# Optimization experiments

Measured on AMD Instinct MI355X. Metric: run time of the kernel, lower is better.

Reference implementation:

```python
import jax, jax.numpy as jnp
import numpy as np

NC, ND = 1024, 64        # computation nodes, device nodes
EC, ED = 16384, 1024     # edges in each graph
FC, FD = 128, 32         # raw feature dims
H = 1024                 # num_hidden
RH = 256                 # num_rnn_hidden


def gconv(feat, src, dst, n_nodes, W, b, act):
    """DGL GraphConv with edge-feature concat (edge feat == ones[E,1])."""
    e = src.shape[0]
    ones_e = jnp.ones((e,), feat.dtype)
    out_deg = jnp.clip(jax.ops.segment_sum(ones_e, src, num_segments=n_nodes), 1.0)
    feat_n = feat * (out_deg ** -0.5)[:, None]
    # sum distributes over concat columns: aggregate src feats and edge feats separately
    h_src = jax.ops.segment_sum(feat_n[src], dst, num_segments=n_nodes)      # [N, in]
    h_e = jax.ops.segment_sum(ones_e, dst, num_segments=n_nodes)[:, None]    # [N, 1]
    h = jnp.concatenate([h_src, h_e], axis=1)                                 # [N, in+1]
    rst = h @ W
    in_deg = jnp.clip(jax.ops.segment_sum(ones_e, dst, num_segments=n_nodes), 1.0)
    rst = rst * (in_deg ** -0.5)[:, None] + b
    return act(rst) if act is not None else rst


def gru_dir(x, Wx, Wh, b, reverse):
    """Keras GRU (reset_after=True), x: [B,T,D] -> [B,T,H]."""
    B = x.shape[0]
    h_dim = Wh.shape[0]
    b_in, b_rec = b[0], b[1]
    xp = jnp.einsum('btd,dh->bth', x, Wx) + b_in   # [B,T,3H]
    xs = jnp.swapaxes(xp, 0, 1)                    # [T,B,3H]
    if reverse:
        xs = xs[::-1]

    def step(h, xt):
        rec = h @ Wh + b_rec
        xz, xr, xh = jnp.split(xt, 3, axis=-1)
        rz, rr, rh = jnp.split(rec, 3, axis=-1)
        z = jax.nn.sigmoid(xz + rz)
        r = jax.nn.sigmoid(xr + rr)
        hh = jnp.tanh(xh + r * rh)
        h_new = z * h + (1.0 - z) * hh
        return h_new, h_new

    h0 = jnp.zeros((B, h_dim), x.dtype)
    _, ys = jax.lax.scan(step, h0, xs)
    if reverse:
        ys = ys[::-1]
    return jnp.swapaxes(ys, 0, 1)


def setup_inputs() -> dict:
    key = jax.random.key(0)
    ks = jax.random.split(key, 20)
    s = 0.05
    return {
        'comp_feat': jax.random.normal(ks[0], (NC, FC), jnp.float32),
        'dev_feat': jax.random.normal(ks[1], (ND, FD), jnp.float32),
        'comp_src': jax.random.randint(ks[2], (EC,), 0, NC, jnp.int32),
        'comp_dst': jax.random.randint(ks[3], (EC,), 0, NC, jnp.int32),
        'dev_src': jax.random.randint(ks[4], (ED,), 0, ND, jnp.int32),
        'dev_dst': jax.random.randint(ks[5], (ED,), 0, ND, jnp.int32),
        'W1c': jax.random.normal(ks[6], (FC + 1, H), jnp.float32) * s,
        'b1c': jnp.zeros((H,), jnp.float32),
        'W2c': jax.random.normal(ks[7], (H + 1, H), jnp.float32) * s,
        'b2c': jnp.zeros((H,), jnp.float32),
        'W1d': jax.random.normal(ks[8], (FD + 1, H), jnp.float32) * s,
        'b1d': jnp.zeros((H,), jnp.float32),
        'W2d': jax.random.normal(ks[9], (H + 1, H), jnp.float32) * s,
        'b2d': jnp.zeros((H,), jnp.float32),
        'Wx_f': jax.random.normal(ks[10], (2 * H, 3 * RH), jnp.float32) * s,
        'Wh_f': jax.random.normal(ks[11], (RH, 3 * RH), jnp.float32) * s,
        'b_f': jnp.zeros((2, 3 * RH), jnp.float32),
        'Wx_b': jax.random.normal(ks[12], (2 * H, 3 * RH), jnp.float32) * s,
        'Wh_b': jax.random.normal(ks[13], (RH, 3 * RH), jnp.float32) * s,
        'b_b': jnp.zeros((2, 3 * RH), jnp.float32),
        'Wf': jax.random.normal(ks[14], (2 * RH, 3), jnp.float32) * s,
        'bf': jnp.zeros((3,), jnp.float32),
    }


def reference(comp_feat, dev_feat, comp_src, comp_dst, dev_src, dev_dst,
              W1c, b1c, W2c, b2c, W1d, b1d, W2d, b2d,
              Wx_f, Wh_f, b_f, Wx_b, Wh_b, b_b, Wf, bf):
    # computation graph GConv stack
    x = gconv(comp_feat, comp_src, comp_dst, NC, W1c, b1c, jax.nn.elu)
    comp_emb = gconv(x, comp_src, comp_dst, NC, W2c, b2c, None)          # [NC, H]
    # device graph GConv stack
    x = gconv(dev_feat, dev_src, dev_dst, ND, W1d, b1d, jax.nn.elu)
    dev_emb = gconv(x, dev_src, dev_dst, ND, W2d, b2d, None)             # [ND, H]
    # pairwise concat: [NC, ND, 2H]
    c = jnp.broadcast_to(comp_emb[:, None, :], (NC, ND, H))
    d = jnp.broadcast_to(dev_emb[None, :, :], (NC, ND, H))
    x = jnp.concatenate([c, d], axis=-1)
    # bidirectional GRU over device axis
    yf = gru_dir(x, Wx_f, Wh_f, b_f, reverse=False)
    yb = gru_dir(x, Wx_b, Wh_b, b_b, reverse=True)
    y = jnp.concatenate([yf, yb], axis=-1)                               # [NC, ND, 2*RH]
    return jax.nn.log_softmax(y @ Wf + bf, axis=-1)                      # [NC, ND, 3]
```

## Files before the change

kernel.cpp:

```cpp
#include <hip/hip_runtime.h>
#include <math.h>

#define NCN 1024
#define NDN 64
#define ECE 16384
#define EDE 1024
#define FCF 128
#define FDF 32
#define HDIM 1024
#define RH 256
#define NG 768
#define TT 64

#define OFF_DEG_OC 0
#define OFF_DEG_IC 1024
#define OFF_DEG_OD 2048
#define OFF_DEG_ID 2112
#define OFF_AGG_C  2176
#define SZ_AGG_C   (1024*1028)
#define OFF_X1C    (OFF_AGG_C + SZ_AGG_C)
#define OFF_EMB_C  (OFF_X1C + 1024*1024)
#define OFF_AGG_D  (OFF_EMB_C + 1024*1024)
#define SZ_AGG_D   (64*1028)
#define OFF_X1D    (OFF_AGG_D + SZ_AGG_D)
#define OFF_EMB_D  (OFF_X1D + 64*1024)
#define OFF_AX     (OFF_EMB_D + 64*1024)
#define OFF_DX     (OFF_AX + 2*1024*768)
#define OFF_WHB    (OFF_DX + 2*64*768)

#define EPI_NONE 0
#define EPI_BIAS 1
#define EPI_GCONV 2
#define EPI_GCONV_ELU 3

typedef __attribute__((ext_vector_type(8))) short s16x8;
typedef __attribute__((ext_vector_type(4))) float f32x4;

__device__ __forceinline__ unsigned short bf16rne(float x) {
    unsigned u = __float_as_uint(x);
    return (unsigned short)((u + 0x7FFFu + ((u >> 16) & 1u)) >> 16);
}

__global__ void fill_k(float* p, int n, float v) {
    int i = blockIdx.x * blockDim.x + threadIdx.x;
    int stride = gridDim.x * blockDim.x;
    for (; i < n; i += stride) p[i] = v;
}

__global__ void degree_k(const int* __restrict__ csrc, const int* __restrict__ cdst,
                         const int* __restrict__ dsrc, const int* __restrict__ ddst,
                         float* ws) {
    int i = blockIdx.x * blockDim.x + threadIdx.x;
    if (i < ECE) {
        atomicAdd(&ws[OFF_DEG_OC + csrc[i]], 1.0f);
        atomicAdd(&ws[OFF_DEG_IC + cdst[i]], 1.0f);
    } else if (i < ECE + EDE) {
        int e = i - ECE;
        atomicAdd(&ws[OFF_DEG_OD + dsrc[e]], 1.0f);
        atomicAdd(&ws[OFF_DEG_ID + ddst[e]], 1.0f);
    }
}

__global__ void agg_k(const float* __restrict__ feat, int F, int logF,
                      const int* __restrict__ src, const int* __restrict__ dst,
                      int E, const float* __restrict__ degout,
                      float* __restrict__ agg, int lda) {
    int i = blockIdx.x * blockDim.x + threadIdx.x;
    int total = E << logF;
    if (i >= total) return;
    int e = i >> logF;
    int f = i & (F - 1);
    int s = src[e];
    float nv = feat[(s << logF) + f] * rsqrtf(fmaxf(degout[s], 1.0f));
    atomicAdd(&agg[dst[e] * lda + f], nv);
}

__global__ void degcol_k(float* agg, int lda, int F, const float* __restrict__ degin, int n) {
    int i = blockIdx.x * blockDim.x + threadIdx.x;
    if (i < n) agg[i * lda + F] = degin[i];
}

__global__ __launch_bounds__(256)
void gemm_k(const float* __restrict__ A, int lda,
            const float* __restrict__ B, int ldb,
            float* __restrict__ C, int ldc,
            int M, int N, int K, int epi,
            const float* __restrict__ scale, const float* __restrict__ bias) {
    __shared__ float As[16][68];
    __shared__ float Bs[16][64];
    int t = threadIdx.x;
    int tx = t & 15, ty = t >> 4;
    int row0 = blockIdx.y * 64, col0 = blockIdx.x * 64;
    int ar = t & 63, ac4 = t >> 6;
    int bk = t >> 4, bc4 = t & 15;
    float acc[4][4] = {};
    int ktiles = (K + 15) >> 4;
    bool avec = ((lda & 3) == 0);
    for (int kt = 0; kt < ktiles; ++kt) {
        int k0 = kt << 4;
        bool full = (k0 + 16 <= K);
        if (full && avec) {
            float4 av = *(const float4*)(A + (size_t)(row0 + ar) * lda + k0 + ac4 * 4);
            As[ac4 * 4 + 0][ar] = av.x; As[ac4 * 4 + 1][ar] = av.y;
            As[ac4 * 4 + 2][ar] = av.z; As[ac4 * 4 + 3][ar] = av.w;
        } else {
#pragma unroll
            for (int j = 0; j < 4; ++j) {
                int kc = k0 + ac4 * 4 + j;
                As[ac4 * 4 + j][ar] = (kc < K) ? A[(size_t)(row0 + ar) * lda + kc] : 0.0f;
            }
        }
        if (full) {
            float4 bv = *(const float4*)(B + (size_t)(k0 + bk) * ldb + col0 + bc4 * 4);
            *(float4*)&Bs[bk][bc4 * 4] = bv;
        } else {
            int kr = k0 + bk;
#pragma unroll
            for (int j = 0; j < 4; ++j)
                Bs[bk][bc4 * 4 + j] = (kr < K) ? B[(size_t)kr * ldb + col0 + bc4 * 4 + j] : 0.0f;
        }
        __syncthreads();
#pragma unroll
        for (int kk = 0; kk < 16; ++kk) {
            float4 a = *(const float4*)&As[kk][ty * 4];
            float4 b = *(const float4*)&Bs[kk][tx * 4];
            acc[0][0] += a.x * b.x; acc[0][1] += a.x * b.y; acc[0][2] += a.x * b.z; acc[0][3] += a.x * b.w;
            acc[1][0] += a.y * b.x; acc[1][1] += a.y * b.y; acc[1][2] += a.y * b.z; acc[1][3] += a.y * b.w;
            acc[2][0] += a.z * b.x; acc[2][1] += a.z * b.y; acc[2][2] += a.z * b.z; acc[2][3] += a.z * b.w;
            acc[3][0] += a.w * b.x; acc[3][1] += a.w * b.y; acc[3][2] += a.w * b.z; acc[3][3] += a.w * b.w;
        }
        __syncthreads();
    }
#pragma unroll
    for (int i = 0; i < 4; ++i) {
#pragma unroll
        for (int j = 0; j < 4; ++j) {
            int r = row0 + ty * 4 + i, c = col0 + tx * 4 + j;
            if (r < M && c < N) {
                float v = acc[i][j];
                if (epi == EPI_BIAS) v += bias[c];
                else if (epi >= EPI_GCONV) {
                    v = v * rsqrtf(fmaxf(scale[r], 1.0f)) + bias[c];
                    if (epi == EPI_GCONV_ELU) v = (v > 0.0f) ? v : expm1f(v);
                }
                C[(size_t)r * ldc + c] = v;
            }
        }
    }
}

__global__ void whb_k(const float* __restrict__ Whf, const float* __restrict__ Whb,
                      unsigned short* __restrict__ whB) {
    int i = blockIdx.x * blockDim.x + threadIdx.x;
    if (i >= 2 * 48 * 8 * 64) return;
    int lane = i & 63;
    int kt = (i >> 6) & 7;
    int nt = (i >> 9) % 48;
    int dir = i / (48 * 8 * 64);
    const float* W = dir ? Whb : Whf;
    int col = nt * 16 + (lane & 15);
    int k0 = kt * 32 + ((lane >> 4) << 3);
    unsigned short* o = whB + (size_t)i * 8;
#pragma unroll
    for (int j = 0; j < 8; ++j)
        o[j] = bf16rne(W[(size_t)(k0 + j) * 768 + col]);
}

__global__ __launch_bounds__(512, 1)
void scan_k(const float* __restrict__ AX, const float* __restrict__ DX,
            const unsigned short* __restrict__ whB,
            const float* __restrict__ b_f, const float* __restrict__ b_b,
            const float* __restrict__ Wf, float* __restrict__ out) {
    __shared__ unsigned short aL[8 * 64 * 8];
    __shared__ float recL[8 * 776];
    int wg = blockIdx.x;
    int dir = wg >> 7;
    int rg = wg & 127;
    int tid = threadIdx.x;
    int lane = tid & 63, wv = tid >> 6;
    int c = tid & 255, rh = tid >> 8, mb = rh * 4;

    const float* brec = (dir ? b_b : b_f) + 768;
    const float* dxb = DX + (size_t)dir * 64 * 768;
    const unsigned short* wB = whB + (size_t)dir * 48 * 8 * 512
                                   + (size_t)wv * 6 * 8 * 512 + (size_t)lane * 8;

    float ax[4][3];
#pragma unroll
    for (int rr = 0; rr < 4; ++rr) {
        const float* arow = AX + ((size_t)dir * 1024 + rg * 8 + mb + rr) * 768;
#pragma unroll
        for (int g = 0; g < 3; ++g) ax[rr][g] = arow[g * 256 + c];
    }
    float br[3];
#pragma unroll
    for (int g = 0; g < 3; ++g) br[g] = brec[g * 256 + c];
    float wf[3];
#pragma unroll
    for (int j = 0; j < 3; ++j) wf[j] = Wf[(dir * 256 + c) * 3 + j];
    float hold[4] = {0.0f, 0.0f, 0.0f, 0.0f};

    for (int i = tid; i < 8 * 64 * 8; i += 512) aL[i] = 0;
    __syncthreads();

    int ab = (c >> 5) * 512 + ((c >> 3) & 3) * 128 + (c & 7);

    for (int s = 0; s < 64; ++s) {
        int t = dir ? (63 - s) : s;

        s16x8 af[8];
#pragma unroll
        for (int kt = 0; kt < 8; ++kt)
            af[kt] = *(const s16x8*)&aL[(kt * 64 + lane) * 8];
#pragma unroll
        for (int n = 0; n < 6; ++n) {
            f32x4 acc = {0.0f, 0.0f, 0.0f, 0.0f};
            const unsigned short* bp = wB + (size_t)n * 8 * 512;
#pragma unroll
            for (int kt = 0; kt < 8; ++kt) {
                s16x8 bfrag = *(const s16x8*)(bp + (size_t)kt * 512);
                acc = __builtin_amdgcn_mfma_f32_16x16x32_bf16(af[kt], bfrag, acc, 0, 0, 0);
            }
            if (lane < 32) {
                int r0 = (lane >> 4) * 4;
                int col = (wv * 6 + n) * 16 + (lane & 15);
#pragma unroll
                for (int r = 0; r < 4; ++r)
                    recL[(r0 + r) * 776 + col] = acc[r];
            }
        }
        __syncthreads();

        const float* dxr = dxb + (size_t)t * 768;
        float dx0 = dxr[c], dx1 = dxr[256 + c], dx2 = dxr[512 + c];
        float p[4][3];
#pragma unroll
        for (int rr = 0; rr < 4; ++rr) {
            int r = mb + rr;
            float rz = recL[r * 776 + c];
            float rr_ = recL[r * 776 + 256 + c];
            float rhh = recL[r * 776 + 512 + c];
            float z   = 1.0f / (1.0f + expf(-(ax[rr][0] + dx0 + rz + br[0])));
            float rg_ = 1.0f / (1.0f + expf(-(ax[rr][1] + dx1 + rr_ + br[1])));
            float hh  = tanhf(ax[rr][2] + dx2 + rg_ * (rhh + br[2]));
            float hn = z * hold[rr] + (1.0f - z) * hh;
            hold[rr] = hn;
            aL[ab + r * 8] = bf16rne(hn);
            p[rr][0] = hn * wf[0]; p[rr][1] = hn * wf[1]; p[rr][2] = hn * wf[2];
        }
#pragma unroll
        for (int off = 32; off; off >>= 1)
#pragma unroll
            for (int rr = 0; rr < 4; ++rr)
#pragma unroll
                for (int j = 0; j < 3; ++j)
                    p[rr][j] += __shfl_down(p[rr][j], off);
        if ((tid & 63) == 0) {
#pragma unroll
            for (int rr = 0; rr < 4; ++rr) {
                int b = rg * 8 + mb + rr;
                float* o = out + ((size_t)b * 64 + t) * 3;
                atomicAdd(&o[0], p[rr][0]);
                atomicAdd(&o[1], p[rr][1]);
                atomicAdd(&o[2], p[rr][2]);
            }
        }
        __syncthreads();
    }
}

__global__ void initout_k(float* out, const float* __restrict__ bf) {
    int i = blockIdx.x * blockDim.x + threadIdx.x;
    if (i < NCN * TT) {
        out[3 * i + 0] = bf[0];
        out[3 * i + 1] = bf[1];
        out[3 * i + 2] = bf[2];
    }
}

__global__ void lsm_k(float* out) {
    int i = blockIdx.x * blockDim.x + threadIdx.x;
    if (i >= NCN * TT) return;
    float v0 = out[3 * i], v1 = out[3 * i + 1], v2 = out[3 * i + 2];
    float m = fmaxf(v0, fmaxf(v1, v2));
    float l = m + logf(expf(v0 - m) + expf(v1 - m) + expf(v2 - m));
    out[3 * i] = v0 - l; out[3 * i + 1] = v1 - l; out[3 * i + 2] = v2 - l;
}

extern "C" void kernel_launch(void* const* d_in, const int* in_sizes, int n_in,
                              void* d_out, int out_size, void* d_ws, size_t ws_size,
                              hipStream_t stream) {
    const float* comp_feat = (const float*)d_in[0];
    const float* dev_feat  = (const float*)d_in[1];
    const int* comp_src = (const int*)d_in[2];
    const int* comp_dst = (const int*)d_in[3];
    const int* dev_src  = (const int*)d_in[4];
    const int* dev_dst  = (const int*)d_in[5];
    const float* W1c = (const float*)d_in[6];  const float* b1c = (const float*)d_in[7];
    const float* W2c = (const float*)d_in[8];  const float* b2c = (const float*)d_in[9];
    const float* W1d = (const float*)d_in[10]; const float* b1d = (const float*)d_in[11];
    const float* W2d = (const float*)d_in[12]; const float* b2d = (const float*)d_in[13];
    const float* Wx_f = (const float*)d_in[14]; const float* Wh_f = (const float*)d_in[15];
    const float* b_f  = (const float*)d_in[16];
    const float* Wx_b = (const float*)d_in[17]; const float* Wh_b = (const float*)d_in[18];
    const float* b_b  = (const float*)d_in[19];
    const float* Wf = (const float*)d_in[20];  const float* bf = (const float*)d_in[21];
    float* out = (float*)d_out;
    float* ws = (float*)d_ws;

    fill_k<<<16, 256, 0, stream>>>(ws, 2176, 0.0f);
    fill_k<<<4096, 256, 0, stream>>>(ws + OFF_AGG_C, SZ_AGG_C, 0.0f);
    fill_k<<<256, 256, 0, stream>>>(ws + OFF_AGG_D, SZ_AGG_D, 0.0f);

    degree_k<<<(ECE + EDE + 255) / 256, 256, 0, stream>>>(comp_src, comp_dst, dev_src, dev_dst, ws);

    agg_k<<<(ECE * FCF + 255) / 256, 256, 0, stream>>>(comp_feat, FCF, 7, comp_src, comp_dst, ECE,
                                                       ws + OFF_DEG_OC, ws + OFF_AGG_C, 132);
    agg_k<<<(EDE * FDF + 255) / 256, 256, 0, stream>>>(dev_feat, FDF, 5, dev_src, dev_dst, EDE,
                                                       ws + OFF_DEG_OD, ws + OFF_AGG_D, 36);
    degcol_k<<<4, 256, 0, stream>>>(ws + OFF_AGG_C, 132, FCF, ws + OFF_DEG_IC, NCN);
    degcol_k<<<1, 64, 0, stream>>>(ws + OFF_AGG_D, 36, FDF, ws + OFF_DEG_ID, NDN);

    gemm_k<<<dim3(16, 16), 256, 0, stream>>>(ws + OFF_AGG_C, 132, W1c, HDIM,
                                             ws + OFF_X1C, HDIM, NCN, HDIM, FCF + 1,
                                             EPI_GCONV_ELU, ws + OFF_DEG_IC, b1c);
    gemm_k<<<dim3(16, 1), 256, 0, stream>>>(ws + OFF_AGG_D, 36, W1d, HDIM,
                                            ws + OFF_X1D, HDIM, NDN, HDIM, FDF + 1,
                                            EPI_GCONV_ELU, ws + OFF_DEG_ID, b1d);

    fill_k<<<4096, 256, 0, stream>>>(ws + OFF_AGG_C, SZ_AGG_C, 0.0f);
    fill_k<<<256, 256, 0, stream>>>(ws + OFF_AGG_D, SZ_AGG_D, 0.0f);
    agg_k<<<(ECE * HDIM + 255) / 256, 256, 0, stream>>>(ws + OFF_X1C, HDIM, 10, comp_src, comp_dst, ECE,
                                                        ws + OFF_DEG_OC, ws + OFF_AGG_C, 1028);
    agg_k<<<(EDE * HDIM + 255) / 256, 256, 0, stream>>>(ws + OFF_X1D, HDIM, 10, dev_src, dev_dst, EDE,
                                                        ws + OFF_DEG_OD, ws + OFF_AGG_D, 1028);
    degcol_k<<<4, 256, 0, stream>>>(ws + OFF_AGG_C, 1028, HDIM, ws + OFF_DEG_IC, NCN);
    degcol_k<<<1, 64, 0, stream>>>(ws + OFF_AGG_D, 1028, HDIM, ws + OFF_DEG_ID, NDN);

    gemm_k<<<dim3(16, 16), 256, 0, stream>>>(ws + OFF_AGG_C, 1028, W2c, HDIM,
                                             ws + OFF_EMB_C, HDIM, NCN, HDIM, HDIM + 1,
                                             EPI_GCONV, ws + OFF_DEG_IC, b2c);
    gemm_k<<<dim3(16, 1), 256, 0, stream>>>(ws + OFF_AGG_D, 1028, W2d, HDIM,
                                            ws + OFF_EMB_D, HDIM, NDN, HDIM, HDIM + 1,
                                            EPI_GCONV, ws + OFF_DEG_ID, b2d);

    gemm_k<<<dim3(12, 16), 256, 0, stream>>>(ws + OFF_EMB_C, HDIM, Wx_f, NG,
                                             ws + OFF_AX, NG, NCN, NG, HDIM,
                                             EPI_NONE, nullptr, nullptr);
    gemm_k<<<dim3(12, 16), 256, 0, stream>>>(ws + OFF_EMB_C, HDIM, Wx_b, NG,
                                             ws + OFF_AX + 1024 * 768, NG, NCN, NG, HDIM,
                                             EPI_NONE, nullptr, nullptr);
    gemm_k<<<dim3(12, 1), 256, 0, stream>>>(ws + OFF_EMB_D, HDIM, Wx_f + 1024 * 768, NG,
                                            ws + OFF_DX, NG, NDN, NG, HDIM,
                                            EPI_BIAS, nullptr, b_f);
    gemm_k<<<dim3(12, 1), 256, 0, stream>>>(ws + OFF_EMB_D, HDIM, Wx_b + 1024 * 768, NG,
                                            ws + OFF_DX + 64 * 768, NG, NDN, NG, HDIM,
                                            EPI_BIAS, nullptr, b_b);

    whb_k<<<(2 * 48 * 8 * 64 + 255) / 256, 256, 0, stream>>>(Wh_f, Wh_b,
                                                             (unsigned short*)(ws + OFF_WHB));
    initout_k<<<256, 256, 0, stream>>>(out, bf);
    scan_k<<<256, 512, 0, stream>>>(ws + OFF_AX, ws + OFF_DX,
                                    (const unsigned short*)(ws + OFF_WHB),
                                    b_f, b_b, Wf, out);
    lsm_k<<<256, 256, 0, stream>>>(out);
}
```

Before: 1.113 ms.

## Keep recurrent weight fragments in registers and stage input projections in LDS

The scan kernel now loads all 48 bf16 B-fragments of the recurrent weight matrix into registers once, before the 64-step loop, so they are no longer re-read from global memory on every step. To make room for those registers, the per-thread input-projection values move into shared memory (axL), and the A fragments are read from LDS inside the k loop rather than preloaded. The launch bound now requests 2 blocks per CU. The 192 VGPRs of weight fragments plus that occupancy target may force register spills, and the extra LDS traffic adds latency inside the serial recurrence.

```diff
diff --git a/kernel.cpp b/kernel.cpp
--- a/kernel.cpp
+++ b/kernel.cpp
@@ -166,13 +166,14 @@
         o[j] = bf16rne(W[(size_t)(k0 + j) * 768 + col]);
 }
 
-__global__ __launch_bounds__(512, 1)
+__global__ __launch_bounds__(512, 2)
 void scan_k(const float* __restrict__ AX, const float* __restrict__ DX,
             const unsigned short* __restrict__ whB,
             const float* __restrict__ b_f, const float* __restrict__ b_b,
             const float* __restrict__ Wf, float* __restrict__ out) {
     __shared__ unsigned short aL[8 * 64 * 8];
     __shared__ float recL[8 * 776];
+    __shared__ float axL[8 * 768];
     int wg = blockIdx.x;
     int dir = wg >> 7;
     int rg = wg & 127;
@@ -182,16 +183,21 @@
 
     const float* brec = (dir ? b_b : b_f) + 768;
     const float* dxb = DX + (size_t)dir * 64 * 768;
-    const unsigned short* wB = whB + (size_t)dir * 48 * 8 * 512
-                                   + (size_t)wv * 6 * 8 * 512 + (size_t)lane * 8;
-
-    float ax[4][3];
-#pragma unroll
-    for (int rr = 0; rr < 4; ++rr) {
-        const float* arow = AX + ((size_t)dir * 1024 + rg * 8 + mb + rr) * 768;
-#pragma unroll
-        for (int g = 0; g < 3; ++g) ax[rr][g] = arow[g * 256 + c];
-    }
+
+    s16x8 bfr[48];
+    {
+        const unsigned short* wB = whB + (size_t)dir * 48 * 8 * 512
+                                       + (size_t)wv * 6 * 8 * 512 + (size_t)lane * 8;
+#pragma unroll
+        for (int f = 0; f < 48; ++f)
+            bfr[f] = *(const s16x8*)(wB + (size_t)f * 512);
+    }
+
+    {
+        const float* axg = AX + ((size_t)dir * 1024 + rg * 8) * 768;
+        for (int i = tid; i < 8 * 768; i += 512) axL[i] = axg[i];
+    }
+
     float br[3];
 #pragma unroll
     for (int g = 0; g < 3; ++g) br[g] = brec[g * 256 + c];
@@ -208,18 +214,13 @@
     for (int s = 0; s < 64; ++s) {
         int t = dir ? (63 - s) : s;
 
-        s16x8 af[8];
-#pragma unroll
-        for (int kt = 0; kt < 8; ++kt)
-            af[kt] = *(const s16x8*)&aL[(kt * 64 + lane) * 8];
 #pragma unroll
         for (int n = 0; n < 6; ++n) {
             f32x4 acc = {0.0f, 0.0f, 0.0f, 0.0f};
-            const unsigned short* bp = wB + (size_t)n * 8 * 512;
 #pragma unroll
             for (int kt = 0; kt < 8; ++kt) {
-                s16x8 bfrag = *(const s16x8*)(bp + (size_t)kt * 512);
-                acc = __builtin_amdgcn_mfma_f32_16x16x32_bf16(af[kt], bfrag, acc, 0, 0, 0);
+                s16x8 af = *(const s16x8*)&aL[(kt * 64 + lane) * 8];
+                acc = __builtin_amdgcn_mfma_f32_16x16x32_bf16(af, bfr[n * 8 + kt], acc, 0, 0, 0);
             }
             if (lane < 32) {
                 int r0 = (lane >> 4) * 4;
@@ -237,12 +238,15 @@
 #pragma unroll
         for (int rr = 0; rr < 4; ++rr) {
             int r = mb + rr;
-            float rz = recL[r * 776 + c];
+            float a0 = axL[r * 768 + c];
+            float a1 = axL[r * 768 + 256 + c];
+            float a2 = axL[r * 768 + 512 + c];
+            float rz  = recL[r * 776 + c];
             float rr_ = recL[r * 776 + 256 + c];
             float rhh = recL[r * 776 + 512 + c];
-            float z   = 1.0f / (1.0f + expf(-(ax[rr][0] + dx0 + rz + br[0])));
-            float rg_ = 1.0f / (1.0f + expf(-(ax[rr][1] + dx1 + rr_ + br[1])));
-            float hh  = tanhf(ax[rr][2] + dx2 + rg_ * (rhh + br[2]));
+            float z   = 1.0f / (1.0f + expf(-(a0 + dx0 + rz + br[0])));
+            float rg_ = 1.0f / (1.0f + expf(-(a1 + dx1 + rr_ + br[1])));
+            float hh  = tanhf(a2 + dx2 + rg_ * (rhh + br[2]));
             float hn = z * hold[rr] + (1.0f - z) * hh;
             hold[rr] = hn;
             aL[ab + r * 8] = bf16rne(hn);
```

Measured after the change: 1.055 ms. 1.05x faster.
